# Performance work log

Measured on AMD Instinct MI355X. Metric: run time of the kernel, lower is better.

Reference implementation:

```python
import jax, jax.numpy as jnp
import numpy as np

G_W = 16  # side of output glimpse patches
K = 3     # number of scales
S = 2     # scale factor between successive patches


def setup_inputs() -> dict:
    key = jax.random.key(0)
    k1, k2 = jax.random.split(key)
    img = jax.random.normal(k1, (256, 224, 224, 3), dtype=jnp.float32)
    # normalized fixation locations in [-1, 1]; (-1,-1)=upper-left, (1,1)=lower-right
    loc = jax.random.uniform(k2, (256, 2), dtype=jnp.float32, minval=-1.0, maxval=1.0)
    return {"img": img, "loc": loc}


def reference(img, loc):
    """Multi-scale glimpse sensor rho(img, loc).

    For each scale i in [0, K), extracts a (g_w * s**i) square patch centered at
    loc (after padding so patches never run off the image), then bilinearly
    resizes it to (g_w, g_w). Returns (B, K, g_w, g_w, C).
    """
    B, H, W, C = img.shape
    max_d = G_W * S ** (K - 1)          # largest patch side (64)
    pad = max_d // 2
    padded = jnp.pad(img, ((0, 0), (pad, pad), (pad, pad), (0, 0)))

    # normalized [-1,1] -> pixel coords of fixation center
    cy = jnp.floor((loc[:, 0] + 1.0) * 0.5 * H).astype(jnp.int32)
    cx = jnp.floor((loc[:, 1] + 1.0) * 0.5 * W).astype(jnp.int32)
    cy = jnp.clip(cy, 0, H)
    cx = jnp.clip(cx, 0, W)

    patches = []
    for i in range(K):
        d = G_W * S ** i                # patch side at this scale
        y0 = cy + pad - d // 2          # top-left corner in padded coords, (B,)
        x0 = cx + pad - d // 2

        def extract(im, y, x, d=d, C=C):
            return jax.lax.dynamic_slice(im, (y, x, 0), (d, d, C))

        p = jax.vmap(extract)(padded, y0, x0)               # (B, d, d, C)
        p = jax.image.resize(p, (B, G_W, G_W, C), method="bilinear")
        patches.append(p)

    return jnp.stack(patches, axis=1)   # (B, K, G_W, G_W, C)
```

## Files before the change

### kernel.cpp

```cpp
#include <hip/hip_runtime.h>
#include <math.h>


#define IMG_H 224
#define IMG_W 224
#define ROWF  672
#define RS2   193
#define RS1   97

struct F3 { float x, y, z; };

__device__ __forceinline__ F3 ld3(const float* p) {
  return *(const F3*)p;
}

__global__ __launch_bounds__(512) void glimpse_kernel(
    const float* __restrict__ img, const float* __restrict__ loc,
    float* __restrict__ out) {
  __shared__ float v2[16 * RS2];
  __shared__ float v1[16 * RS1];

  const int b = blockIdx.x;
  const int tid = threadIdx.x;

  const float ly = loc[b * 2 + 0];
  const float lx = loc[b * 2 + 1];
  int cy = (int)floorf((ly + 1.0f) * 0.5f * (float)IMG_H);
  int cx = (int)floorf((lx + 1.0f) * 0.5f * (float)IMG_W);
  cy = min(max(cy, 0), IMG_H);
  cx = min(max(cx, 0), IMG_W);
  const int oy0 = cy - 32;
  const int ox0 = cx - 32;

  const float* imgb = img + (size_t)b * IMG_H * ROWF;

  float wb2[8], wb1[4];
#pragma unroll
  for (int t = 0; t < 8; ++t) wb2[t] = 1.0f - fabsf((float)t - 3.5f) * 0.25f;
#pragma unroll
  for (int t = 0; t < 4; ++t) wb1[t] = 1.0f - fabsf((float)t - 1.5f) * 0.5f;

#pragma unroll
  for (int it = 0; it < 2; ++it) {
    const int task = it * 512 + tid;
    const int x = task & 63;
    const int i = task >> 6;
    const int ky0 = 4 * i - 2;
    const int xx = ox0 + x;
    const int xc = min(max(xx, 0), IMG_W - 1);
    const float fx = ((unsigned)xx < IMG_W) ? 1.0f : 0.f;
    float a0 = 0.f, a1 = 0.f, a2 = 0.f;
#pragma unroll
    for (int t = 0; t < 8; ++t) {
      const int ky = ky0 + t;
      const int yy = oy0 + ky;
      const float we =
          (((unsigned)ky < 64u) && ((unsigned)yy < IMG_H)) ? wb2[t] * fx : 0.f;
      const int yc = min(max(yy, 0), IMG_H - 1);
      const F3 p = ld3(imgb + (size_t)yc * ROWF + (size_t)xc * 3);
      a0 = fmaf(we, p.x, a0);
      a1 = fmaf(we, p.y, a1);
      a2 = fmaf(we, p.z, a2);
    }
    const float rsy = (i == 0 || i == 15) ? (1.0f / 3.5f) : 0.25f;
    const int w = i * RS2 + 3 * x;
    v2[w + 0] = a0 * rsy;
    v2[w + 1] = a1 * rsy;
    v2[w + 2] = a2 * rsy;
  }

  {
    const int x = tid & 31;
    const int i = tid >> 5;
    const int ky0 = 2 * i - 1;
    const int xx = ox0 + 16 + x;
    const int xc = min(max(xx, 0), IMG_W - 1);
    const float fx = ((unsigned)xx < IMG_W) ? 1.0f : 0.f;
    float a0 = 0.f, a1 = 0.f, a2 = 0.f;
#pragma unroll
    for (int t = 0; t < 4; ++t) {
      const int ky = ky0 + t;
      const int yy = oy0 + 16 + ky;
      const float we =
          (((unsigned)ky < 32u) && ((unsigned)yy < IMG_H)) ? wb1[t] * fx : 0.f;
      const int yc = min(max(yy, 0), IMG_H - 1);
      const F3 p = ld3(imgb + (size_t)yc * ROWF + (size_t)xc * 3);
      a0 = fmaf(we, p.x, a0);
      a1 = fmaf(we, p.y, a1);
      a2 = fmaf(we, p.z, a2);
    }
    const float rsy = (i == 0 || i == 15) ? (1.0f / 1.75f) : 0.5f;
    const int w = i * RS1 + 3 * x;
    v1[w + 0] = a0 * rsy;
    v1[w + 1] = a1 * rsy;
    v1[w + 2] = a2 * rsy;
  }

  if (tid < 256) {
    const int jy = tid >> 4;
    const int jx = tid & 15;
    const int yy = oy0 + 24 + jy;
    const int xx = ox0 + 24 + jx;
    const float we =
        (((unsigned)yy < IMG_H) && ((unsigned)xx < IMG_W)) ? 1.0f : 0.f;
    const int yc = min(max(yy, 0), IMG_H - 1);
    const int xc = min(max(xx, 0), IMG_W - 1);
    const F3 p = ld3(imgb + (size_t)yc * ROWF + (size_t)xc * 3);
    float* o = out + ((size_t)(b * 3 + 0) * 256 + tid) * 3;
    o[0] = we * p.x;
    o[1] = we * p.y;
    o[2] = we * p.z;
  }

  __syncthreads();

  if (tid < 256) {
    const int jy = tid >> 4;
    const int jx = tid & 15;
    const int kx0 = 4 * jx - 2;
    float a0 = 0.f, a1 = 0.f, a2 = 0.f;
#pragma unroll
    for (int t = 0; t < 8; ++t) {
      const int kx = kx0 + t;
      const float we = ((unsigned)kx < 64u) ? wb2[t] : 0.f;
      const int kc = min(max(kx, 0), 63);
      const int base = jy * RS2 + 3 * kc;
      a0 = fmaf(we, v2[base + 0], a0);
      a1 = fmaf(we, v2[base + 1], a1);
      a2 = fmaf(we, v2[base + 2], a2);
    }
    const float rsx = (jx == 0 || jx == 15) ? (1.0f / 3.5f) : 0.25f;
    float* o = out + ((size_t)(b * 3 + 2) * 256 + tid) * 3;
    o[0] = a0 * rsx;
    o[1] = a1 * rsx;
    o[2] = a2 * rsx;
  } else {
    const int px = tid - 256;
    const int jy = px >> 4;
    const int jx = px & 15;
    const int kx0 = 2 * jx - 1;
    float a0 = 0.f, a1 = 0.f, a2 = 0.f;
#pragma unroll
    for (int t = 0; t < 4; ++t) {
      const int kx = kx0 + t;
      const float we = ((unsigned)kx < 32u) ? wb1[t] : 0.f;
      const int kc = min(max(kx, 0), 31);
      const int base = jy * RS1 + 3 * kc;
      a0 = fmaf(we, v1[base + 0], a0);
      a1 = fmaf(we, v1[base + 1], a1);
      a2 = fmaf(we, v1[base + 2], a2);
    }
    const float rsx = (jx == 0 || jx == 15) ? (1.0f / 1.75f) : 0.5f;
    float* o = out + ((size_t)(b * 3 + 1) * 256 + px) * 3;
    o[0] = a0 * rsx;
    o[1] = a1 * rsx;
    o[2] = a2 * rsx;
  }
}

extern "C" void kernel_launch(void* const* d_in, const int* in_sizes, int n_in,
                              void* d_out, int out_size, void* d_ws, size_t ws_size,
                              hipStream_t stream) {
  const float* img = (const float*)d_in[0];
  const float* loc = (const float*)d_in[1];
  float* out = (float*)d_out;
  const int B = in_sizes[1] / 2;
  glimpse_kernel<<<B, 512, 0, stream>>>(img, loc, out);
}
```

Baseline: 9.858 us.

## Stage full 64x64 patch in shared memory and compute all scales from it

After: 9.866 us. Within noise of the previous version (+0.1%).

```diff
diff --git a/kernel.cpp b/kernel.cpp
--- a/kernel.cpp
+++ b/kernel.cpp
@@ -5,19 +5,17 @@
 #define IMG_H 224
 #define IMG_W 224
 #define ROWF  672
-#define RS2   193
+#define RSP   193
 #define RS1   97
 
 struct F3 { float x, y, z; };
+__device__ __forceinline__ F3 ld3(const float* p) { return *(const F3*)p; }
 
-__device__ __forceinline__ F3 ld3(const float* p) {
-  return *(const F3*)p;
-}
-
-__global__ __launch_bounds__(512) void glimpse_kernel(
+__global__ __launch_bounds__(1024, 1) void glimpse_kernel(
     const float* __restrict__ img, const float* __restrict__ loc,
     float* __restrict__ out) {
-  __shared__ float v2[16 * RS2];
+  __shared__ float patch[64 * RSP];
+  __shared__ float v2[16 * RSP];
   __shared__ float v1[16 * RS1];
 
   const int b = blockIdx.x;
@@ -41,53 +39,60 @@
   for (int t = 0; t < 4; ++t) wb1[t] = 1.0f - fabsf((float)t - 1.5f) * 0.5f;
 
 #pragma unroll
-  for (int it = 0; it < 2; ++it) {
-    const int task = it * 512 + tid;
+  for (int it = 0; it < 4; ++it) {
+    const int task = it * 1024 + tid;
     const int x = task & 63;
-    const int i = task >> 6;
+    const int row = task >> 6;
+    const int yy = oy0 + row;
+    const int xx = ox0 + x;
+    const float we =
+        (((unsigned)yy < IMG_H) && ((unsigned)xx < IMG_W)) ? 1.0f : 0.f;
+    const int yc = min(max(yy, 0), IMG_H - 1);
+    const int xc = min(max(xx, 0), IMG_W - 1);
+    const F3 p = ld3(imgb + (size_t)yc * ROWF + (size_t)xc * 3);
+    const int w = row * RSP + 3 * x;
+    patch[w + 0] = we * p.x;
+    patch[w + 1] = we * p.y;
+    patch[w + 2] = we * p.z;
+  }
+  __syncthreads();
+
+  {
+    const int x = tid & 63;
+    const int i = tid >> 6;
     const int ky0 = 4 * i - 2;
-    const int xx = ox0 + x;
-    const int xc = min(max(xx, 0), IMG_W - 1);
-    const float fx = ((unsigned)xx < IMG_W) ? 1.0f : 0.f;
     float a0 = 0.f, a1 = 0.f, a2 = 0.f;
 #pragma unroll
     for (int t = 0; t < 8; ++t) {
       const int ky = ky0 + t;
-      const int yy = oy0 + ky;
-      const float we =
-          (((unsigned)ky < 64u) && ((unsigned)yy < IMG_H)) ? wb2[t] * fx : 0.f;
-      const int yc = min(max(yy, 0), IMG_H - 1);
-      const F3 p = ld3(imgb + (size_t)yc * ROWF + (size_t)xc * 3);
-      a0 = fmaf(we, p.x, a0);
-      a1 = fmaf(we, p.y, a1);
-      a2 = fmaf(we, p.z, a2);
+      const float we = ((unsigned)ky < 64u) ? wb2[t] : 0.f;
+      const int kc = min(max(ky, 0), 63);
+      const int base = kc * RSP + 3 * x;
+      a0 = fmaf(we, patch[base + 0], a0);
+      a1 = fmaf(we, patch[base + 1], a1);
+      a2 = fmaf(we, patch[base + 2], a2);
     }
     const float rsy = (i == 0 || i == 15) ? (1.0f / 3.5f) : 0.25f;
-    const int w = i * RS2 + 3 * x;
+    const int w = i * RSP + 3 * x;
     v2[w + 0] = a0 * rsy;
     v2[w + 1] = a1 * rsy;
     v2[w + 2] = a2 * rsy;
   }
 
-  {
+  if (tid < 512) {
     const int x = tid & 31;
     const int i = tid >> 5;
     const int ky0 = 2 * i - 1;
-    const int xx = ox0 + 16 + x;
-    const int xc = min(max(xx, 0), IMG_W - 1);
-    const float fx = ((unsigned)xx < IMG_W) ? 1.0f : 0.f;
     float a0 = 0.f, a1 = 0.f, a2 = 0.f;
 #pragma unroll
     for (int t = 0; t < 4; ++t) {
       const int ky = ky0 + t;
-      const int yy = oy0 + 16 + ky;
-      const float we =
-          (((unsigned)ky < 32u) && ((unsigned)yy < IMG_H)) ? wb1[t] * fx : 0.f;
-      const int yc = min(max(yy, 0), IMG_H - 1);
-      const F3 p = ld3(imgb + (size_t)yc * ROWF + (size_t)xc * 3);
-      a0 = fmaf(we, p.x, a0);
-      a1 = fmaf(we, p.y, a1);
-      a2 = fmaf(we, p.z, a2);
+      const float we = ((unsigned)ky < 32u) ? wb1[t] : 0.f;
+      const int kc = min(max(ky, 0), 31);
+      const int base = (16 + kc) * RSP + 3 * (16 + x);
+      a0 = fmaf(we, patch[base + 0], a0);
+      a1 = fmaf(we, patch[base + 1], a1);
+      a2 = fmaf(we, patch[base + 2], a2);
     }
     const float rsy = (i == 0 || i == 15) ? (1.0f / 1.75f) : 0.5f;
     const int w = i * RS1 + 3 * x;
@@ -96,20 +101,15 @@
     v1[w + 2] = a2 * rsy;
   }
 
-  if (tid < 256) {
-    const int jy = tid >> 4;
-    const int jx = tid & 15;
-    const int yy = oy0 + 24 + jy;
-    const int xx = ox0 + 24 + jx;
-    const float we =
-        (((unsigned)yy < IMG_H) && ((unsigned)xx < IMG_W)) ? 1.0f : 0.f;
-    const int yc = min(max(yy, 0), IMG_H - 1);
-    const int xc = min(max(xx, 0), IMG_W - 1);
-    const F3 p = ld3(imgb + (size_t)yc * ROWF + (size_t)xc * 3);
-    float* o = out + ((size_t)(b * 3 + 0) * 256 + tid) * 3;
-    o[0] = we * p.x;
-    o[1] = we * p.y;
-    o[2] = we * p.z;
+  if (tid >= 512 && tid < 768) {
+    const int px = tid - 512;
+    const int jy = px >> 4;
+    const int jx = px & 15;
+    const int base = (24 + jy) * RSP + 3 * (24 + jx);
+    float* o = out + ((size_t)(b * 3 + 0) * 256 + px) * 3;
+    o[0] = patch[base + 0];
+    o[1] = patch[base + 1];
+    o[2] = patch[base + 2];
   }
 
   __syncthreads();
@@ -124,7 +124,7 @@
       const int kx = kx0 + t;
       const float we = ((unsigned)kx < 64u) ? wb2[t] : 0.f;
       const int kc = min(max(kx, 0), 63);
-      const int base = jy * RS2 + 3 * kc;
+      const int base = jy * RSP + 3 * kc;
       a0 = fmaf(we, v2[base + 0], a0);
       a1 = fmaf(we, v2[base + 1], a1);
       a2 = fmaf(we, v2[base + 2], a2);
@@ -134,7 +134,7 @@
     o[0] = a0 * rsx;
     o[1] = a1 * rsx;
     o[2] = a2 * rsx;
-  } else {
+  } else if (tid < 512) {
     const int px = tid - 256;
     const int jy = px >> 4;
     const int jx = px & 15;
@@ -165,5 +165,5 @@
   const float* loc = (const float*)d_in[1];
   float* out = (float*)d_out;
   const int B = in_sizes[1] / 2;
-  glimpse_kernel<<<B, 512, 0, stream>>>(img, loc, out);
+  glimpse_kernel<<<B, 1024, 0, stream>>>(img, loc, out);
 }
```
